# Kernel optimization log

Measured on AMD Instinct MI355X. Metric: run time of the kernel, lower is better.

Reference implementation:

```python
import jax, jax.numpy as jnp
import numpy as np

B, D, K, H, E, Z = 64, 25000, 16, 128, 256, 32


def setup_inputs() -> dict:
    key = jax.random.key(0)
    ks = jax.random.split(key, 10)
    s = 0.02
    return {
        "x": jax.random.normal(ks[0], (B, D), jnp.float32),
        "mask": jax.random.randint(ks[1], (B, D), 0, 2, jnp.int32),
        "feat_emb": jax.random.normal(ks[2], (D, K), jnp.float32),          # feature_embedding [D,K]
        "feat_bias": jnp.zeros((D, 1), jnp.float32),                        # feature_bias [D,1]
        "W1": jax.random.normal(ks[3], (1 + K + 1, H), jnp.float32) * s,    # h_layer linear 1 (in,out)
        "b1": jnp.zeros((H,), jnp.float32),
        "W2": jax.random.normal(ks[4], (H, K), jnp.float32) * s,            # h_layer linear 2
        "b2": jnp.zeros((K,), jnp.float32),
        "We1": jax.random.normal(ks[5], (K, E), jnp.float32) * s,           # encoder_mlp linear 1
        "be1": jnp.zeros((E,), jnp.float32),
        "We2": jax.random.normal(ks[6], (E, 2 * Z), jnp.float32) * s,       # encoder_mlp linear 2
        "be2": jnp.zeros((2 * Z,), jnp.float32),
    }


def reference(x, mask, feat_emb, feat_bias, W1, b1, W2, b2, We1, be1, We2, be2):
    b, d = x.shape
    k = feat_emb.shape[1]
    # Build per-(sample, feature) input rows: [x_bd, F_d(K), bias_d] -> [B, D, 1+K+1]
    h_in = jnp.concatenate(
        [
            x[:, :, None],
            jnp.broadcast_to(feat_emb[None, :, :], (b, d, k)),
            jnp.broadcast_to(feat_bias[None, :, :], (b, d, 1)),
        ],
        axis=-1,
    )
    # Shared small MLP (h_layer), dropout is identity at rate 0.0
    h = jax.nn.relu(h_in @ W1 + b1)          # [B, D, H]
    h = jax.nn.relu(h @ W2 + b2)             # [B, D, K]
    # Masked sum pooling over features
    c = jnp.sum(h * mask.astype(h.dtype)[:, :, None], axis=1)  # [B, K]
    # encoder_mlp
    enc = jax.nn.relu(c @ We1 + be1) @ We2 + be2                # [B, 2Z]
    mu, logvar = jnp.split(enc, 2, axis=-1)
    return mu, logvar
```

## Files before the change

kernel.cpp:

```cpp
#include <hip/hip_runtime.h>

#define B 64
#define D 25000
#define K 16
#define H 128
#define E 256
#define Z 32
#define DTILE 16
#define NT_TILES ((D + DTILE - 1) / DTILE)
#define NPB 512
#define XROW 20
#define MROWF 68

typedef __attribute__((ext_vector_type(8))) _Float16 half8;
typedef __attribute__((ext_vector_type(4))) _Float16 hv4;
typedef __attribute__((ext_vector_type(2))) _Float16 hv2;
typedef __attribute__((ext_vector_type(4))) float f32x4;

__global__ __launch_bounds__(256, 2) void main_kernel(
    const float* __restrict__ x, const int* __restrict__ mask,
    const float* __restrict__ feat_emb, const float* __restrict__ feat_bias,
    const float* __restrict__ W1, const float* __restrict__ b1,
    const float* __restrict__ W2, const float* __restrict__ b2,
    float* __restrict__ part)
{
    __shared__ __align__(16) _Float16 sGh[2][DTILE * H];
    __shared__ __align__(16) _Float16 sXb[2][B * XROW];
    __shared__ __align__(16) float    sMf[2][DTILE * MROWF];
    __shared__ __align__(16) float    sRed[4][B * K];

    const int t    = threadIdx.x;
    const int lane = t & 63;
    const int wv   = t >> 6;
    const int g    = lane >> 4;
    const int n    = lane & 15;

    half8 Bf[4];
    #pragma unroll
    for (int s = 0; s < 4; ++s) {
        union { half8 v; _Float16 e[8]; } u;
        #pragma unroll
        for (int j = 0; j < 8; ++j)
            u.e[j] = (_Float16)W2[(s * 32 + g * 8 + j) * K + n];
        Bf[s] = u.v;
    }
    hv2 w0h[4][4];
    #pragma unroll
    for (int s = 0; s < 4; ++s) {
        const float4* wp = (const float4*)&W1[s * 32 + g * 8];
        float4 a0 = wp[0], a1 = wp[1];
        w0h[s][0] = (hv2){(_Float16)a0.x, (_Float16)a0.y};
        w0h[s][1] = (hv2){(_Float16)a0.z, (_Float16)a0.w};
        w0h[s][2] = (hv2){(_Float16)a1.x, (_Float16)a1.y};
        w0h[s][3] = (hv2){(_Float16)a1.z, (_Float16)a1.w};
    }
    half8 bfG[2];
    #pragma unroll
    for (int cc = 0; cc < 2; ++cc) {
        const int h = (wv * 2 + cc) * 16 + n;
        union { half8 v; _Float16 e[8]; } u;
        #pragma unroll
        for (int j = 0; j < 8; ++j) {
            const int k = g * 8 + j;
            float v;
            if (k < 16)       v = W1[(1 + k) * H + h];
            else if (k == 16) v = W1[17 * H + h];
            else if (k == 17) v = b1[h];
            else              v = 0.f;
            u.e[j] = (_Float16)v;
        }
        bfG[cc] = u.v;
    }
    const float b2n = b2[n];
    const hv2 zeroh = {(_Float16)0.f, (_Float16)0.f};
    const int ddb = wv * 4;

    auto STAGE = [&](int buf, int tile) {
        const int bb = t >> 2;
        const int dd = (t & 3) * 4;
        const int dg = tile * DTILE + dd;
        float xv[4], mv[4];
        if (dg + 4 <= D) {
            float4 xx = *(const float4*)&x[(size_t)bb * D + dg];
            int4   mm = *(const int4*)&mask[(size_t)bb * D + dg];
            xv[0] = xx.x; xv[1] = xx.y; xv[2] = xx.z; xv[3] = xx.w;
            mv[0] = (float)mm.x; mv[1] = (float)mm.y; mv[2] = (float)mm.z; mv[3] = (float)mm.w;
        } else {
            #pragma unroll
            for (int i = 0; i < 4; ++i) {
                const int dgi = dg + i;
                xv[i] = (dgi < D) ? x[(size_t)bb * D + dgi] : 0.f;
                mv[i] = (dgi < D) ? (float)mask[(size_t)bb * D + dgi] : 0.f;
            }
        }
        hv4 xp = {(_Float16)xv[0], (_Float16)xv[1], (_Float16)xv[2], (_Float16)xv[3]};
        *(hv4*)&sXb[buf][bb * XROW + dd] = xp;
        #pragma unroll
        for (int i = 0; i < 4; ++i)
            sMf[buf][(dd + i) * MROWF + bb] = mv[i];
    };

    auto GCOMP = [&](int buf, int tile) {
        const int dA = min(tile * DTILE + n, D - 1);
        union { half8 v; _Float16 e[8]; } af;
        if (g < 2) {
            const float4* fe = (const float4*)&feat_emb[(size_t)dA * K + g * 8];
            float4 u0 = fe[0], u1 = fe[1];
            af.e[0] = (_Float16)u0.x; af.e[1] = (_Float16)u0.y;
            af.e[2] = (_Float16)u0.z; af.e[3] = (_Float16)u0.w;
            af.e[4] = (_Float16)u1.x; af.e[5] = (_Float16)u1.y;
            af.e[6] = (_Float16)u1.z; af.e[7] = (_Float16)u1.w;
        } else if (g == 2) {
            af.e[0] = (_Float16)feat_bias[dA];
            af.e[1] = (_Float16)1.f;
            #pragma unroll
            for (int j = 2; j < 8; ++j) af.e[j] = (_Float16)0.f;
        } else {
            #pragma unroll
            for (int j = 0; j < 8; ++j) af.e[j] = (_Float16)0.f;
        }
        #pragma unroll
        for (int cc = 0; cc < 2; ++cc) {
            f32x4 C = {0.f, 0.f, 0.f, 0.f};
            C = __builtin_amdgcn_mfma_f32_16x16x32_f16(af.v, bfG[cc], C, 0, 0, 0);
            #pragma unroll
            for (int r = 0; r < 4; ++r)
                sGh[buf][(g * 4 + r) * H + (wv * 2 + cc) * 16 + n] = (_Float16)C[r];
        }
    };

    f32x4 cacc[4] = {{0.f,0.f,0.f,0.f},{0.f,0.f,0.f,0.f},{0.f,0.f,0.f,0.f},{0.f,0.f,0.f,0.f}};

    int tt = blockIdx.x;
    STAGE(0, tt);
    GCOMP(0, tt);
    __syncthreads();

    int cur = 0;
    for (; tt < NT_TILES; tt += NPB) {
        const int nxt = tt + NPB;
        if (nxt < NT_TILES) { STAGE(cur ^ 1, nxt); GCOMP(cur ^ 1, nxt); }

        hv4 xq[4];
        #pragma unroll
        for (int m = 0; m < 4; ++m)
            xq[m] = *(const hv4*)&sXb[cur][(m * 16 + n) * XROW + ddb];

        #pragma unroll
        for (int i = 0; i < 4; ++i) {
            const int dd = ddb + i;
            half8 Gv[4];
            #pragma unroll
            for (int s = 0; s < 4; ++s)
                Gv[s] = *(const half8*)&sGh[cur][dd * H + s * 32 + g * 8];
            #pragma unroll
            for (int m = 0; m < 4; ++m) {
                const _Float16 xs = xq[m][i];
                const hv2 xx = {xs, xs};
                f32x4 c1 = {b2n, b2n, b2n, b2n};
                #pragma unroll
                for (int s = 0; s < 4; ++s) {
                    union GA { half8 v; hv2 p[4]; };
                    GA gg, A0;
                    gg.v = Gv[s];
                    #pragma unroll
                    for (int p = 0; p < 4; ++p) {
                        hv2 h0 = __builtin_elementwise_fma(xx, w0h[s][p], gg.p[p]);
                        A0.p[p] = __builtin_elementwise_max(h0, zeroh);
                    }
                    c1 = __builtin_amdgcn_mfma_f32_16x16x32_f16(A0.v, Bf[s], c1, 0, 0, 0);
                }
                float4 mk = *(const float4*)&sMf[cur][dd * MROWF + m * 16 + g * 4];
                cacc[m][0] = fmaf(mk.x, fmaxf(c1[0], 0.f), cacc[m][0]);
                cacc[m][1] = fmaf(mk.y, fmaxf(c1[1], 0.f), cacc[m][1]);
                cacc[m][2] = fmaf(mk.z, fmaxf(c1[2], 0.f), cacc[m][2]);
                cacc[m][3] = fmaf(mk.w, fmaxf(c1[3], 0.f), cacc[m][3]);
            }
        }
        __syncthreads();
        cur ^= 1;
    }

    #pragma unroll
    for (int m = 0; m < 4; ++m)
        #pragma unroll
        for (int r = 0; r < 4; ++r)
            sRed[wv][(m * 16 + g * 4 + r) * K + n] = cacc[m][r];
    __syncthreads();
    #pragma unroll
    for (int q = 0; q < 4; ++q) {
        const int o = t + q * 256;
        const float v = sRed[0][o] + sRed[1][o] + sRed[2][o] + sRed[3][o];
        part[(size_t)(o >> 4) * (NPB * K) + (size_t)blockIdx.x * K + (o & 15)] = v;
    }
}

__global__ __launch_bounds__(256) void partial_enc_kernel(
    const float* __restrict__ part, const float* __restrict__ We1,
    const float* __restrict__ be1, const float* __restrict__ We2,
    const float* __restrict__ be2, float* __restrict__ out)
{
    const int b = blockIdx.x;
    const int t = threadIdx.x;
    __shared__ float sc[K];
    __shared__ float st1[E];
    __shared__ float red[256];

    {
        const float* pb = part + (size_t)b * (NPB * K);
        float acc0 = 0.f;
        #pragma unroll 8
        for (int i = 0; i < (NPB * K) / 256; ++i)
            acc0 += pb[t + i * 256];
        red[t] = acc0;
    }
    __syncthreads();
    if (t < K) {
        float s2 = 0.f;
        #pragma unroll
        for (int q = 0; q < 16; ++q) s2 += red[q * 16 + t];
        sc[t] = s2;
    }
    __syncthreads();

    {
        float acc = be1[t];
        #pragma unroll
        for (int k = 0; k < K; ++k)
            acc = fmaf(sc[k], We1[k * E + t], acc);
        st1[t] = fmaxf(acc, 0.f);
    }
    __syncthreads();

    const int j = t & 63, seg = t >> 6;
    float acc = 0.f;
    #pragma unroll 4
    for (int e = seg * 64; e < seg * 64 + 64; ++e)
        acc = fmaf(st1[e], We2[e * 64 + j], acc);
    red[t] = acc;
    __syncthreads();

    if (t < 64) {
        float v = red[j] + red[64 + j] + red[128 + j] + red[192 + j] + be2[j];
        if (j < Z) out[b * Z + j] = v;
        else       out[B * Z + b * Z + (j - Z)] = v;
    }
}

extern "C" void kernel_launch(void* const* d_in, const int* in_sizes, int n_in,
                              void* d_out, int out_size, void* d_ws, size_t ws_size,
                              hipStream_t stream) {
    const float* x         = (const float*)d_in[0];
    const int*   mask      = (const int*)  d_in[1];
    const float* feat_emb  = (const float*)d_in[2];
    const float* feat_bias = (const float*)d_in[3];
    const float* W1        = (const float*)d_in[4];
    const float* b1        = (const float*)d_in[5];
    const float* W2        = (const float*)d_in[6];
    const float* b2        = (const float*)d_in[7];
    const float* We1       = (const float*)d_in[8];
    const float* be1       = (const float*)d_in[9];
    const float* We2       = (const float*)d_in[10];
    const float* be2       = (const float*)d_in[11];

    float* part = (float*)d_ws;

    main_kernel<<<NPB, 256, 0, stream>>>(
        x, mask, feat_emb, feat_bias, W1, b1, W2, b2, part);
    partial_enc_kernel<<<B, 256, 0, stream>>>(
        part, We1, be1, We2, be2, (float*)d_out);
}
```

Baseline: 108.4 us.

## Fuse encoder MLP into main kernel via atomic completion counter

Merges the second launch into the main kernel. Each block increments a global counter after writing its partials, and the last 64 blocks spin until all 512 blocks are done before running the reduction and encoder MLP. This removes one kernel launch and the gap between launches, but adds a memset, a spin-wait, and a reliance on all 512 blocks being co-resident or already retired (512 blocks at 2 per CU fits on 256 CUs).

```diff
diff --git a/kernel.cpp b/kernel.cpp
--- a/kernel.cpp
+++ b/kernel.cpp
@@ -17,17 +17,22 @@
 typedef __attribute__((ext_vector_type(2))) _Float16 hv2;
 typedef __attribute__((ext_vector_type(4))) float f32x4;
 
-__global__ __launch_bounds__(256, 2) void main_kernel(
+__global__ __launch_bounds__(256, 2) void fused_kernel(
     const float* __restrict__ x, const int* __restrict__ mask,
     const float* __restrict__ feat_emb, const float* __restrict__ feat_bias,
     const float* __restrict__ W1, const float* __restrict__ b1,
     const float* __restrict__ W2, const float* __restrict__ b2,
-    float* __restrict__ part)
+    const float* __restrict__ We1, const float* __restrict__ be1,
+    const float* __restrict__ We2, const float* __restrict__ be2,
+    float* __restrict__ part, unsigned* __restrict__ ctr,
+    float* __restrict__ out)
 {
     __shared__ __align__(16) _Float16 sGh[2][DTILE * H];
     __shared__ __align__(16) _Float16 sXb[2][B * XROW];
     __shared__ __align__(16) float    sMf[2][DTILE * MROWF];
     __shared__ __align__(16) float    sRed[4][B * K];
+    __shared__ float sc[K];
+    __shared__ float st1[E];
 
     const int t    = threadIdx.x;
     const int lane = t & 63;
@@ -193,32 +198,36 @@
         const float v = sRed[0][o] + sRed[1][o] + sRed[2][o] + sRed[3][o];
         part[(size_t)(o >> 4) * (NPB * K) + (size_t)blockIdx.x * K + (o & 15)] = v;
     }
-}
-
-__global__ __launch_bounds__(256) void partial_enc_kernel(
-    const float* __restrict__ part, const float* __restrict__ We1,
-    const float* __restrict__ be1, const float* __restrict__ We2,
-    const float* __restrict__ be2, float* __restrict__ out)
-{
-    const int b = blockIdx.x;
-    const int t = threadIdx.x;
-    __shared__ float sc[K];
-    __shared__ float st1[E];
-    __shared__ float red[256];
+
+    __syncthreads();
+    if (t == 0) {
+        __threadfence();
+        atomicAdd(ctr, 1u);
+    }
+
+    const int eb = (int)blockIdx.x - (NPB - B);
+    if (eb < 0) return;
+
+    if (t == 0) {
+        while (__hip_atomic_load(ctr, __ATOMIC_ACQUIRE, __HIP_MEMORY_SCOPE_AGENT) < NPB)
+            __builtin_amdgcn_s_sleep(16);
+        __threadfence();
+    }
+    __syncthreads();
 
     {
-        const float* pb = part + (size_t)b * (NPB * K);
+        const float* pb = part + (size_t)eb * (NPB * K);
         float acc0 = 0.f;
         #pragma unroll 8
         for (int i = 0; i < (NPB * K) / 256; ++i)
             acc0 += pb[t + i * 256];
-        red[t] = acc0;
+        sRed[0][t] = acc0;
     }
     __syncthreads();
     if (t < K) {
         float s2 = 0.f;
         #pragma unroll
-        for (int q = 0; q < 16; ++q) s2 += red[q * 16 + t];
+        for (int q = 0; q < 16; ++q) s2 += sRed[0][q * 16 + t];
         sc[t] = s2;
     }
     __syncthreads();
@@ -237,13 +246,13 @@
     #pragma unroll 4
     for (int e = seg * 64; e < seg * 64 + 64; ++e)
         acc = fmaf(st1[e], We2[e * 64 + j], acc);
-    red[t] = acc;
+    sRed[0][t] = acc;
     __syncthreads();
 
     if (t < 64) {
-        float v = red[j] + red[64 + j] + red[128 + j] + red[192 + j] + be2[j];
-        if (j < Z) out[b * Z + j] = v;
-        else       out[B * Z + b * Z + (j - Z)] = v;
+        float v = sRed[0][j] + sRed[0][64 + j] + sRed[0][128 + j] + sRed[0][192 + j] + be2[j];
+        if (j < Z) out[eb * Z + j] = v;
+        else       out[B * Z + eb * Z + (j - Z)] = v;
     }
 }
 
@@ -263,10 +272,11 @@
     const float* We2       = (const float*)d_in[10];
     const float* be2       = (const float*)d_in[11];
 
-    float* part = (float*)d_ws;
-
-    main_kernel<<<NPB, 256, 0, stream>>>(
-        x, mask, feat_emb, feat_bias, W1, b1, W2, b2, part);
-    partial_enc_kernel<<<B, 256, 0, stream>>>(
-        part, We1, be1, We2, be2, (float*)d_out);
+    float*    part = (float*)d_ws;
+    unsigned* ctr  = (unsigned*)(part + NPB * B * K);
+
+    hipMemsetAsync(ctr, 0, 4, stream);
+    fused_kernel<<<NPB, 256, 0, stream>>>(
+        x, mask, feat_emb, feat_bias, W1, b1, W2, b2,
+        We1, be1, We2, be2, part, ctr, (float*)d_out);
 }
```

Result: slower. 126.0 us (+16.2%).
